# Optimization experiments

Measured on AMD Instinct MI355X. Metric: run time of the kernel, lower is better.

Reference implementation:

```python
import jax, jax.numpy as jnp
import numpy as np

VOXEL = 0.1          # superpoint_voxel_size
NUM_BATCHES = 4      # B (batch indices in coords[:,0] are in [0, B))


def setup_inputs() -> dict:
    key = jax.random.key(0)
    k1, k2, k3, k4, k5, k6, k7 = jax.random.split(key, 7)
    N, D = 1_000_000, 64
    batch_ids = jax.random.randint(k1, (N,), 0, NUM_BATCHES).astype(jnp.float32)
    xyz = jax.random.uniform(k2, (N, 3), dtype=jnp.float32) * 50.0  # 50m scene
    coords = jnp.concatenate([batch_ids[:, None], xyz], axis=1)      # (N,4)
    features = jax.random.normal(k3, (N, D), dtype=jnp.float32)
    s1 = 1.0 / np.sqrt(3.0)
    s2 = 1.0 / np.sqrt(D)
    W1 = jax.random.uniform(k4, (3, D), minval=-s1, maxval=s1, dtype=jnp.float32)
    b1 = jax.random.uniform(k5, (D,), minval=-s1, maxval=s1, dtype=jnp.float32)
    W2 = jax.random.uniform(k6, (D, D), minval=-s2, maxval=s2, dtype=jnp.float32)
    b2 = jax.random.uniform(k7, (D,), minval=-s2, maxval=s2, dtype=jnp.float32)
    return {"coords": coords, "features": features, "W1": W1, "b1": b1, "W2": W2, "b2": b2}


def reference(coords, features, W1, b1, W2, b2):
    N, D = features.shape
    batch_ids = coords[:, 0].astype(jnp.int32)          # (N,)
    xyz = coords[:, 1:4]                                 # (N,3)
    q = jnp.floor(xyz / VOXEL).astype(jnp.int32)         # voxel quantization
    combined = jnp.concatenate([batch_ids[:, None], q], axis=1)  # (N,4) int32 keys

    # torch.unique(dim=0, return_inverse=True): lexicographically sorted unique
    # rows. We pad to a fixed S=N segments (fill rows sorted to the tail via a
    # max sentinel); `valid` masks out the padding.
    SENT = jnp.iinfo(jnp.int32).max
    unique_sp, sp_to_point = jnp.unique(
        combined, axis=0, size=N, fill_value=SENT, return_inverse=True)
    sp_to_point = sp_to_point.reshape(-1)                # (N,)

    counts = jax.ops.segment_sum(jnp.ones((N,), jnp.float32), sp_to_point, num_segments=N)
    valid = counts > 0
    c = jnp.maximum(counts, 1.0)[:, None]                # clamp(min=1)

    sp_features = jax.ops.segment_sum(features, sp_to_point, num_segments=N) / c  # (N,D) mean
    sp_centers = jax.ops.segment_sum(xyz, sp_to_point, num_segments=N) / c        # (N,3) mean

    # pos_enc: Linear(3,D) -> ReLU -> Linear(D,D)
    pos = jnp.maximum(sp_centers @ W1 + b1, 0.0) @ W2 + b2
    sp_features = jnp.where(valid[:, None], sp_features + pos, 0.0)
    sp_centers = jnp.where(valid[:, None], sp_centers, 0.0)

    # batch_offsets: cumulative superpoint counts per batch (padding -> dump bin B)
    sp_batch = jnp.where(valid, unique_sp[:, 0], NUM_BATCHES)
    per_batch = jax.ops.segment_sum(jnp.ones((N,), jnp.int32), sp_batch,
                                    num_segments=NUM_BATCHES + 1)[:NUM_BATCHES]
    batch_offsets = jnp.concatenate([jnp.zeros((1,), jnp.int32), jnp.cumsum(per_batch)])
    return sp_features, sp_centers, sp_to_point, batch_offsets
```

## Files before the change

kernel.cpp:

```cpp
#include <hip/hip_runtime.h>
#include <stdint.h>


static constexpr uint32_t NWORDS = 1u << 24;
static constexpr uint32_t NBLK   = NWORDS / 1024;
static constexpr uint32_t MCAP   = 65536;

typedef __attribute__((ext_vector_type(8))) short short8;
typedef __attribute__((ext_vector_type(4))) float f32x4;

__device__ __forceinline__ short f2bf(float x) {
    union { float f; uint32_t u; } v; v.f = x;
    uint32_t u = v.u;
    uint32_t r = (u + 0x7FFFu + ((u >> 16) & 1u)) >> 16;
    return (short)r;
}

__device__ __forceinline__ uint32_t point_key(float4 c) {
    uint32_t b  = (uint32_t)(int)c.x;
    uint32_t qx = (uint32_t)(int)floorf(c.y / 0.1f);
    uint32_t qy = (uint32_t)(int)floorf(c.z / 0.1f);
    uint32_t qz = (uint32_t)(int)floorf(c.w / 0.1f);
    return (b << 27) | (qx << 18) | (qy << 9) | qz;
}

__global__ void k0_w2t(const float* __restrict__ W2, short* __restrict__ W2T) {
    int t = blockIdx.x * 256 + threadIdx.x;
    if (t < 4096) {
        int col = t >> 6, k = t & 63;
        W2T[col * 64 + k] = f2bf(W2[k * 64 + col]);
    }
}

__global__ void k1_keys(const float4* __restrict__ coords, uint32_t* __restrict__ bitmap, int N) {
    int i = blockIdx.x * blockDim.x + threadIdx.x;
    if (i >= N) return;
    uint32_t key = point_key(coords[i]);
    atomicOr(&bitmap[key >> 5], 1u << (key & 31u));
}

__global__ __launch_bounds__(256) void k2a_blockscan(
        const uint4* __restrict__ bm4, uint16_t* __restrict__ scan4,
        uint32_t* __restrict__ bsum) {
    int t = threadIdx.x;
    int lane = t & 63, wid = t >> 6;
    uint4 v = bm4[(size_t)blockIdx.x * 256 + t];
    uint32_t pc = __popc(v.x) + __popc(v.y) + __popc(v.z) + __popc(v.w);
    uint32_t sc = pc;
    #pragma unroll
    for (int off = 1; off < 64; off <<= 1) {
        uint32_t n = __shfl_up(sc, off);
        if (lane >= off) sc += n;
    }
    __shared__ uint32_t wt[4];
    if (lane == 63) wt[wid] = sc;
    __syncthreads();
    uint32_t wbase = 0;
    #pragma unroll
    for (int w = 0; w < 4; ++w) wbase += (w < wid) ? wt[w] : 0u;
    scan4[(size_t)blockIdx.x * 256 + t] = (uint16_t)(wbase + sc - pc);
    if (t == 255) bsum[blockIdx.x] = wbase + sc;
}

__global__ void k2b_topscan(const uint32_t* __restrict__ bsum, uint32_t* __restrict__ bscan) {
    __shared__ uint32_t s[1024];
    int t = threadIdx.x;
    uint32_t base = (uint32_t)t * 16u;
    const uint4* b4 = (const uint4*)(bsum + base);
    uint32_t sum = 0;
    #pragma unroll
    for (int k = 0; k < 4; ++k) { uint4 v = b4[k]; sum += v.x + v.y + v.z + v.w; }
    s[t] = sum;
    __syncthreads();
    for (int off = 1; off < 1024; off <<= 1) {
        uint32_t v = (t >= off) ? s[t - off] : 0u;
        __syncthreads();
        s[t] += v;
        __syncthreads();
    }
    uint32_t run = s[t] - sum;
    for (int k = 0; k < 16; ++k) { bscan[base + k] = run; run += bsum[base + k]; }
    if (t == 1023) bscan[16384] = run;
}

__global__ void k3a_rank(const float4* __restrict__ coords,
                         uint32_t* __restrict__ ranks,
                         const uint32_t* __restrict__ bitmap,
                         const uint16_t* __restrict__ scan4,
                         const uint32_t* __restrict__ bscan,
                         float* __restrict__ sums,
                         uint32_t* __restrict__ inv,
                         uint32_t* __restrict__ slotmap,
                         uint32_t* __restrict__ mctr,
                         float* __restrict__ out_sp, int N) {
    int i = blockIdx.x * blockDim.x + threadIdx.x;
    if (i >= N) return;
    float4 c = coords[i];
    uint32_t key = point_key(c);
    uint32_t w = key >> 5, bit = key & 31u;
    uint4 q = *(const uint4*)(bitmap + (w & ~3u));
    uint32_t wd[4] = {q.x, q.y, q.z, q.w};
    uint32_t idx = w & 3u;
    uint32_t r = bscan[w >> 10] + (uint32_t)scan4[w >> 2];
    uint32_t cur = 0;
    #pragma unroll
    for (uint32_t j = 0; j < 4; ++j) {
        r += (j < idx) ? __popc(wd[j]) : 0u;
        cur = (j == idx) ? wd[j] : cur;
    }
    r += __popc(cur & ((1u << bit) - 1u));
    ranks[i] = r;
    inv[r] = (uint32_t)i;
    __builtin_nontemporal_store((float)r, out_sp + i);
    float* s4 = sums + 4u * (size_t)r;
    float old = atomicAdd(s4 + 0, 1.0f);
    s4[1] = c.y; s4[2] = c.z; s4[3] = c.w;
    if (old == 1.0f) {
        uint32_t slot = atomicAdd(mctr, 1u);
        if (slot < MCAP) slotmap[r] = slot + 1u;
    }
}

__global__ void k3fix(const float4* __restrict__ coords,
                      const float* __restrict__ features,
                      const uint32_t* __restrict__ ranks,
                      const uint32_t* __restrict__ slotmap,
                      const float4* __restrict__ sums,
                      float* __restrict__ msum,
                      float* __restrict__ mfeat, int N) {
    int i = blockIdx.x * blockDim.x + threadIdx.x;
    if (i >= N) return;
    uint32_t r = ranks[i];
    uint32_t sl = slotmap[r];
    if (sl == 0) return;
    sl -= 1u;
    float cnt = sums[r].x;
    float4 c = coords[i];
    float* m = msum + 4u * (size_t)sl;
    atomicAdd(m + 0, c.y);
    atomicAdd(m + 1, c.z);
    atomicAdd(m + 2, c.w);
    float iv = 1.0f / cnt;
    const float* frow = features + (size_t)i * 64;
    float* orow = mfeat + (size_t)sl * 64;
    #pragma unroll 1
    for (int qq = 0; qq < 64; ++qq) atomicAdd(&orow[qq], frow[qq] * iv);
}

__global__ __launch_bounds__(256) void k5_fused(
        const f32x4* __restrict__ features4,
        const uint32_t* __restrict__ inv,
        const float4* __restrict__ sums,
        const uint32_t* __restrict__ slotmap,
        const float4* __restrict__ msum,
        const f32x4* __restrict__ mfeat4,
        const float* __restrict__ W1, const float* __restrict__ b1,
        const short* __restrict__ W2T, const float* __restrict__ b2,
        f32x4* __restrict__ out_feat4, float* __restrict__ out_cent, int N) {
    int lane = threadIdx.x & 63;
    int rows_base = blockIdx.x * 256 + (threadIdx.x >> 6) * 64;

    int my = rows_base + lane;
    if (my < N) {
        float4 s4 = sums[my];
        float sx = s4.y, sy = s4.z, sz = s4.w;
        if (s4.x > 1.5f) {
            float4 m = msum[slotmap[my] - 1u];
            sx = m.x; sy = m.y; sz = m.z;
        }
        float ic = s4.x > 0.f ? 1.f / s4.x : 0.f;
        __builtin_nontemporal_store(sx * ic, out_cent + 3 * (size_t)my + 0);
        __builtin_nontemporal_store(sy * ic, out_cent + 3 * (size_t)my + 1);
        __builtin_nontemporal_store(sz * ic, out_cent + 3 * (size_t)my + 2);
    }

    float cntg[4], scx[4], scy[4], scz[4];
    #pragma unroll
    for (int g = 0; g < 4; ++g) {
        int rg = rows_base + (g << 4) + (lane & 15);
        int rgc = rg < N ? rg : N - 1;
        float4 sg = sums[rgc];
        cntg[g] = sg.x;
        float sx = sg.y, sy = sg.z, sz = sg.w;
        if (sg.x > 1.5f) {
            float4 m = msum[slotmap[rgc] - 1u];
            sx = m.x; sy = m.y; sz = m.z;
        }
        float ic = sg.x > 0.f ? 1.f / sg.x : 0.f;
        scx[g] = sx * ic; scy[g] = sy * ic; scz[g] = sz * ic;
    }

    f32x4 acc[4][4];
    #pragma unroll
    for (int cg = 0; cg < 4; ++cg) {
        f32x4 bv = ((const f32x4*)b2)[(cg << 2) + (lane >> 4)];
        #pragma unroll
        for (int g = 0; g < 4; ++g)
            acc[g][cg] = bv;
    }

    #pragma unroll
    for (int s = 0; s < 2; ++s) {
        int kb = s * 32 + ((lane >> 4) << 3);
        float4 tx0 = *(const float4*)(W1 + kb),       tx1 = *(const float4*)(W1 + kb + 4);
        float4 ty0 = *(const float4*)(W1 + 64 + kb),  ty1 = *(const float4*)(W1 + 64 + kb + 4);
        float4 tz0 = *(const float4*)(W1 + 128 + kb), tz1 = *(const float4*)(W1 + 128 + kb + 4);
        float4 tb0 = *(const float4*)(b1 + kb),       tb1 = *(const float4*)(b1 + kb + 4);
        float w1x[8] = {tx0.x, tx0.y, tx0.z, tx0.w, tx1.x, tx1.y, tx1.z, tx1.w};
        float w1y[8] = {ty0.x, ty0.y, ty0.z, ty0.w, ty1.x, ty1.y, ty1.z, ty1.w};
        float w1z[8] = {tz0.x, tz0.y, tz0.z, tz0.w, tz1.x, tz1.y, tz1.z, tz1.w};
        float b1v[8] = {tb0.x, tb0.y, tb0.z, tb0.w, tb1.x, tb1.y, tb1.z, tb1.w};

        short8 afrag[4];
        #pragma unroll
        for (int cg = 0; cg < 4; ++cg) {
            int col = (cg << 4) | (lane & 15);
            afrag[cg] = *(const short8*)(W2T + col * 64 + kb);
        }

        #pragma unroll
        for (int g = 0; g < 4; ++g) {
            short8 hf;
            #pragma unroll
            for (int j = 0; j < 8; ++j) {
                float h = fmaf(scz[g], w1z[j], fmaf(scy[g], w1y[j], fmaf(scx[g], w1x[j], b1v[j])));
                hf[j] = f2bf(fmaxf(h, 0.0f));
            }
            #pragma unroll
            for (int cg = 0; cg < 4; ++cg)
                acc[g][cg] = __builtin_amdgcn_mfma_f32_16x16x32_bf16(afrag[cg], hf, acc[g][cg], 0, 0, 0);
        }
    }

    #pragma unroll
    for (int g = 0; g < 4; ++g) {
        int gr = rows_base + (g << 4) + (lane & 15);
        if (gr >= N) continue;
        float cnt = cntg[g];
        f32x4 v[4];
        #pragma unroll
        for (int cg = 0; cg < 4; ++cg) v[cg] = acc[g][cg];
        if (cnt == 0.0f) {
            #pragma unroll
            for (int cg = 0; cg < 4; ++cg) v[cg] = (f32x4){0.f, 0.f, 0.f, 0.f};
        } else if (cnt == 1.0f) {
            size_t fb = (size_t)inv[gr] * 16 + (lane >> 4);
            #pragma unroll
            for (int cg = 0; cg < 4; ++cg) v[cg] += features4[fb + (cg << 2)];
        } else {
            size_t mb = (size_t)(slotmap[gr] - 1u) * 16 + (lane >> 4);
            #pragma unroll
            for (int cg = 0; cg < 4; ++cg) v[cg] += mfeat4[mb + (cg << 2)];
        }
        size_t ob = (size_t)gr * 16 + (lane >> 4);
        #pragma unroll
        for (int cg = 0; cg < 4; ++cg)
            __builtin_nontemporal_store(v[cg], out_feat4 + ob + (cg << 2));
    }
}

__global__ void k6_offsets(const uint32_t* __restrict__ bscan, float* __restrict__ out_off) {
    int t = threadIdx.x;
    if (t < 5) {
        uint32_t v;
        if (t == 0)      v = 0u;
        else if (t == 4) v = bscan[16384];
        else             v = bscan[(uint32_t)t << 12];
        out_off[t] = (float)v;
    }
}

extern "C" void kernel_launch(void* const* d_in, const int* in_sizes, int n_in,
                              void* d_out, int out_size, void* d_ws, size_t ws_size,
                              hipStream_t stream) {
    const float4* coords = (const float4*)d_in[0];
    const float*  feats  = (const float*)d_in[1];
    const float*  W1 = (const float*)d_in[2];
    const float*  b1 = (const float*)d_in[3];
    const float*  W2 = (const float*)d_in[4];
    const float*  b2 = (const float*)d_in[5];
    int N = in_sizes[0] / 4;

    char* ws = (char*)d_ws;
    size_t o = 0;
    uint32_t* bitmap = (uint32_t*)(ws + o); o += (size_t)NWORDS * 4;
    uint16_t* scan4  = (uint16_t*)(ws + o); o += (size_t)(NWORDS / 4) * 2;
    uint32_t* bsum   = (uint32_t*)(ws + o); o += (size_t)NBLK * 4;
    uint32_t* bscan  = (uint32_t*)(ws + o); o += (size_t)(NBLK + 1) * 4;
    o = (o + 15) & ~(size_t)15;
    uint32_t* ranks  = (uint32_t*)(ws + o); o += (size_t)N * 4;
    o = (o + 15) & ~(size_t)15;
    float*    sums   = (float*)(ws + o);    o += (size_t)N * 16;
    uint32_t* inv    = (uint32_t*)(ws + o); o += (size_t)N * 4;
    o = (o + 15) & ~(size_t)15;
    short*    W2T    = (short*)(ws + o);    o += 8192;
    size_t multi_base = o;
    uint32_t* slotmap = (uint32_t*)(ws + o); o += (size_t)N * 4;
    uint32_t* mctr    = (uint32_t*)(ws + o); o += 16;
    float*    msum    = (float*)(ws + o);    o += (size_t)MCAP * 16;
    float*    mfeat   = (float*)(ws + o);    o += (size_t)MCAP * 256;
    size_t multi_size = o - multi_base;

    float* out_feat = (float*)d_out;
    float* out_cent = out_feat + (size_t)N * 64;
    float* out_sp   = out_cent + (size_t)N * 3;
    float* out_off  = out_sp + N;

    hipMemsetAsync(bitmap, 0, (size_t)NWORDS * 4, stream);
    hipMemsetAsync(sums, 0, (size_t)N * 16, stream);
    hipMemsetAsync(ws + multi_base, 0, multi_size, stream);

    int nb = (N + 255) / 256;
    k0_w2t<<<16, 256, 0, stream>>>(W2, W2T);
    k1_keys<<<nb, 256, 0, stream>>>(coords, bitmap, N);
    k2a_blockscan<<<NBLK, 256, 0, stream>>>((const uint4*)bitmap, scan4, bsum);
    k2b_topscan<<<1, 1024, 0, stream>>>(bsum, bscan);
    k3a_rank<<<nb, 256, 0, stream>>>(coords, ranks, bitmap, scan4, bscan, sums, inv,
                                     slotmap, mctr, out_sp, N);
    k3fix<<<nb, 256, 0, stream>>>(coords, feats, ranks, slotmap, (const float4*)sums,
                                  msum, mfeat, N);
    k5_fused<<<nb, 256, 0, stream>>>((const f32x4*)feats, inv, (const float4*)sums,
                                     slotmap, (const float4*)msum, (const f32x4*)mfeat,
                                     W1, b1, W2T, b2, (f32x4*)out_feat, out_cent, N);
    k6_offsets<<<1, 64, 0, stream>>>(bscan, out_off);
}
```

Measured before the change: 347.1 us.

## Replace multi-point slot aggregation with per-superpoint linked lists gathered in fused kernel

Drops the k3fix atomic-accumulation kernel and the slotmap/msum/mfeat buffers. The rank kernel now builds a per-superpoint singly linked list of point indices with atomicExch. The fused kernel walks that list to sum coordinates and features for multi-point voxels. This removes one launch, a large memset and many float atomics. In exchange it adds pointer-chasing gathers with divergent loop lengths and switches output stores from nontemporal to normal stores.

New measurement: 416.5 us. +20.0%, slower.

```diff
diff --git a/kernel.cpp b/kernel.cpp
--- a/kernel.cpp
+++ b/kernel.cpp
@@ -4,7 +4,6 @@
 
 static constexpr uint32_t NWORDS = 1u << 24;
 static constexpr uint32_t NBLK   = NWORDS / 1024;
-static constexpr uint32_t MCAP   = 65536;
 
 typedef __attribute__((ext_vector_type(8))) short short8;
 typedef __attribute__((ext_vector_type(4))) float f32x4;
@@ -84,14 +83,11 @@
 }
 
 __global__ void k3a_rank(const float4* __restrict__ coords,
-                         uint32_t* __restrict__ ranks,
                          const uint32_t* __restrict__ bitmap,
                          const uint16_t* __restrict__ scan4,
                          const uint32_t* __restrict__ bscan,
-                         float* __restrict__ sums,
-                         uint32_t* __restrict__ inv,
-                         uint32_t* __restrict__ slotmap,
-                         uint32_t* __restrict__ mctr,
+                         float* __restrict__ psum,
+                         uint32_t* __restrict__ next,
                          float* __restrict__ out_sp, int N) {
     int i = blockIdx.x * blockDim.x + threadIdx.x;
     if (i >= N) return;
@@ -109,85 +105,69 @@
         cur = (j == idx) ? wd[j] : cur;
     }
     r += __popc(cur & ((1u << bit) - 1u));
-    ranks[i] = r;
-    inv[r] = (uint32_t)i;
-    __builtin_nontemporal_store((float)r, out_sp + i);
-    float* s4 = sums + 4u * (size_t)r;
-    float old = atomicAdd(s4 + 0, 1.0f);
-    s4[1] = c.y; s4[2] = c.z; s4[3] = c.w;
-    if (old == 1.0f) {
-        uint32_t slot = atomicAdd(mctr, 1u);
-        if (slot < MCAP) slotmap[r] = slot + 1u;
-    }
-}
-
-__global__ void k3fix(const float4* __restrict__ coords,
-                      const float* __restrict__ features,
-                      const uint32_t* __restrict__ ranks,
-                      const uint32_t* __restrict__ slotmap,
-                      const float4* __restrict__ sums,
-                      float* __restrict__ msum,
-                      float* __restrict__ mfeat, int N) {
-    int i = blockIdx.x * blockDim.x + threadIdx.x;
-    if (i >= N) return;
-    uint32_t r = ranks[i];
-    uint32_t sl = slotmap[r];
-    if (sl == 0) return;
-    sl -= 1u;
-    float cnt = sums[r].x;
-    float4 c = coords[i];
-    float* m = msum + 4u * (size_t)sl;
-    atomicAdd(m + 0, c.y);
-    atomicAdd(m + 1, c.z);
-    atomicAdd(m + 2, c.w);
-    float iv = 1.0f / cnt;
-    const float* frow = features + (size_t)i * 64;
-    float* orow = mfeat + (size_t)sl * 64;
-    #pragma unroll 1
-    for (int qq = 0; qq < 64; ++qq) atomicAdd(&orow[qq], frow[qq] * iv);
+    out_sp[i] = (float)r;
+    float* p = psum + 8u * (size_t)r;
+    atomicAdd(p, 1.0f);
+    p[1] = c.y; p[2] = c.z; p[3] = c.w;
+    uint32_t old = atomicExch((uint32_t*)(p + 4), (uint32_t)i + 1u);
+    next[i] = old;
 }
 
 __global__ __launch_bounds__(256) void k5_fused(
+        const float4* __restrict__ coords,
         const f32x4* __restrict__ features4,
-        const uint32_t* __restrict__ inv,
-        const float4* __restrict__ sums,
-        const uint32_t* __restrict__ slotmap,
-        const float4* __restrict__ msum,
-        const f32x4* __restrict__ mfeat4,
+        const float4* __restrict__ psum4,
+        const uint32_t* __restrict__ next,
         const float* __restrict__ W1, const float* __restrict__ b1,
         const short* __restrict__ W2T, const float* __restrict__ b2,
         f32x4* __restrict__ out_feat4, float* __restrict__ out_cent, int N) {
     int lane = threadIdx.x & 63;
     int rows_base = blockIdx.x * 256 + (threadIdx.x >> 6) * 64;
 
-    int my = rows_base + lane;
-    if (my < N) {
-        float4 s4 = sums[my];
-        float sx = s4.y, sy = s4.z, sz = s4.w;
-        if (s4.x > 1.5f) {
-            float4 m = msum[slotmap[my] - 1u];
-            sx = m.x; sy = m.y; sz = m.z;
-        }
-        float ic = s4.x > 0.f ? 1.f / s4.x : 0.f;
-        __builtin_nontemporal_store(sx * ic, out_cent + 3 * (size_t)my + 0);
-        __builtin_nontemporal_store(sy * ic, out_cent + 3 * (size_t)my + 1);
-        __builtin_nontemporal_store(sz * ic, out_cent + 3 * (size_t)my + 2);
-    }
-
     float cntg[4], scx[4], scy[4], scz[4];
+    uint32_t headg[4];
     #pragma unroll
     for (int g = 0; g < 4; ++g) {
         int rg = rows_base + (g << 4) + (lane & 15);
         int rgc = rg < N ? rg : N - 1;
-        float4 sg = sums[rgc];
-        cntg[g] = sg.x;
-        float sx = sg.y, sy = sg.z, sz = sg.w;
-        if (sg.x > 1.5f) {
-            float4 m = msum[slotmap[rgc] - 1u];
-            sx = m.x; sy = m.y; sz = m.z;
-        }
-        float ic = sg.x > 0.f ? 1.f / sg.x : 0.f;
+        float4 q0 = psum4[2 * (size_t)rgc];
+        float4 q1 = psum4[2 * (size_t)rgc + 1];
+        float cnt = q0.x;
+        cntg[g] = cnt;
+        headg[g] = __float_as_uint(q1.x);
+        float sx = q0.y, sy = q0.z, sz = q0.w;
+        if (cnt > 1.5f) {
+            sx = 0.f; sy = 0.f; sz = 0.f;
+            uint32_t j = headg[g];
+            while (j) {
+                float4 cc = coords[j - 1u];
+                sx += cc.y; sy += cc.z; sz += cc.w;
+                j = next[j - 1u];
+            }
+        }
+        float ic = cnt > 0.f ? 1.f / cnt : 0.f;
         scx[g] = sx * ic; scy[g] = sy * ic; scz[g] = sz * ic;
+    }
+
+    int my = rows_base + lane;
+    if (my < N) {
+        float4 q0 = psum4[2 * (size_t)my];
+        float4 q1 = psum4[2 * (size_t)my + 1];
+        float cnt = q0.x;
+        float sx = q0.y, sy = q0.z, sz = q0.w;
+        if (cnt > 1.5f) {
+            sx = 0.f; sy = 0.f; sz = 0.f;
+            uint32_t j = __float_as_uint(q1.x);
+            while (j) {
+                float4 cc = coords[j - 1u];
+                sx += cc.y; sy += cc.z; sz += cc.w;
+                j = next[j - 1u];
+            }
+        }
+        float ic = cnt > 0.f ? 1.f / cnt : 0.f;
+        out_cent[3 * (size_t)my + 0] = sx * ic;
+        out_cent[3 * (size_t)my + 1] = sy * ic;
+        out_cent[3 * (size_t)my + 2] = sz * ic;
     }
 
     f32x4 acc[4][4];
@@ -244,18 +224,28 @@
             #pragma unroll
             for (int cg = 0; cg < 4; ++cg) v[cg] = (f32x4){0.f, 0.f, 0.f, 0.f};
         } else if (cnt == 1.0f) {
-            size_t fb = (size_t)inv[gr] * 16 + (lane >> 4);
+            size_t fb = (size_t)(headg[g] - 1u) * 16 + (lane >> 4);
             #pragma unroll
             for (int cg = 0; cg < 4; ++cg) v[cg] += features4[fb + (cg << 2)];
         } else {
-            size_t mb = (size_t)(slotmap[gr] - 1u) * 16 + (lane >> 4);
-            #pragma unroll
-            for (int cg = 0; cg < 4; ++cg) v[cg] += mfeat4[mb + (cg << 2)];
+            f32x4 fs[4];
+            #pragma unroll
+            for (int cg = 0; cg < 4; ++cg) fs[cg] = (f32x4){0.f, 0.f, 0.f, 0.f};
+            uint32_t j = headg[g];
+            while (j) {
+                size_t fb = (size_t)(j - 1u) * 16 + (lane >> 4);
+                #pragma unroll
+                for (int cg = 0; cg < 4; ++cg) fs[cg] += features4[fb + (cg << 2)];
+                j = next[j - 1u];
+            }
+            float iv = 1.0f / cnt;
+            #pragma unroll
+            for (int cg = 0; cg < 4; ++cg) v[cg] += fs[cg] * iv;
         }
         size_t ob = (size_t)gr * 16 + (lane >> 4);
         #pragma unroll
         for (int cg = 0; cg < 4; ++cg)
-            __builtin_nontemporal_store(v[cg], out_feat4 + ob + (cg << 2));
+            out_feat4[ob + (cg << 2)] = v[cg];
     }
 }
 
@@ -287,19 +277,11 @@
     uint16_t* scan4  = (uint16_t*)(ws + o); o += (size_t)(NWORDS / 4) * 2;
     uint32_t* bsum   = (uint32_t*)(ws + o); o += (size_t)NBLK * 4;
     uint32_t* bscan  = (uint32_t*)(ws + o); o += (size_t)(NBLK + 1) * 4;
-    o = (o + 15) & ~(size_t)15;
-    uint32_t* ranks  = (uint32_t*)(ws + o); o += (size_t)N * 4;
-    o = (o + 15) & ~(size_t)15;
-    float*    sums   = (float*)(ws + o);    o += (size_t)N * 16;
-    uint32_t* inv    = (uint32_t*)(ws + o); o += (size_t)N * 4;
+    o = (o + 31) & ~(size_t)31;
+    float*    psum   = (float*)(ws + o);    o += (size_t)N * 32;
+    uint32_t* next   = (uint32_t*)(ws + o); o += (size_t)N * 4;
     o = (o + 15) & ~(size_t)15;
     short*    W2T    = (short*)(ws + o);    o += 8192;
-    size_t multi_base = o;
-    uint32_t* slotmap = (uint32_t*)(ws + o); o += (size_t)N * 4;
-    uint32_t* mctr    = (uint32_t*)(ws + o); o += 16;
-    float*    msum    = (float*)(ws + o);    o += (size_t)MCAP * 16;
-    float*    mfeat   = (float*)(ws + o);    o += (size_t)MCAP * 256;
-    size_t multi_size = o - multi_base;
 
     float* out_feat = (float*)d_out;
     float* out_cent = out_feat + (size_t)N * 64;
@@ -307,20 +289,15 @@
     float* out_off  = out_sp + N;
 
     hipMemsetAsync(bitmap, 0, (size_t)NWORDS * 4, stream);
-    hipMemsetAsync(sums, 0, (size_t)N * 16, stream);
-    hipMemsetAsync(ws + multi_base, 0, multi_size, stream);
+    hipMemsetAsync(psum, 0, (size_t)N * 32, stream);
 
     int nb = (N + 255) / 256;
     k0_w2t<<<16, 256, 0, stream>>>(W2, W2T);
     k1_keys<<<nb, 256, 0, stream>>>(coords, bitmap, N);
     k2a_blockscan<<<NBLK, 256, 0, stream>>>((const uint4*)bitmap, scan4, bsum);
     k2b_topscan<<<1, 1024, 0, stream>>>(bsum, bscan);
-    k3a_rank<<<nb, 256, 0, stream>>>(coords, ranks, bitmap, scan4, bscan, sums, inv,
-                                     slotmap, mctr, out_sp, N);
-    k3fix<<<nb, 256, 0, stream>>>(coords, feats, ranks, slotmap, (const float4*)sums,
-                                  msum, mfeat, N);
-    k5_fused<<<nb, 256, 0, stream>>>((const f32x4*)feats, inv, (const float4*)sums,
-                                     slotmap, (const float4*)msum, (const f32x4*)mfeat,
-                                     W1, b1, W2T, b2, (f32x4*)out_feat, out_cent, N);
+    k3a_rank<<<nb, 256, 0, stream>>>(coords, bitmap, scan4, bscan, psum, next, out_sp, N);
+    k5_fused<<<nb, 256, 0, stream>>>(coords, (const f32x4*)feats, (const float4*)psum,
+                                     next, W1, b1, W2T, b2, (f32x4*)out_feat, out_cent, N);
     k6_offsets<<<1, 64, 0, stream>>>(bscan, out_off);
 }
```
